# Kernel optimization log

Measured on AMD Instinct MI355X. Metric: run time of the kernel, lower is better.

The kernel has to match this reference:

```python
import jax, jax.numpy as jnp
import numpy as np

B, TAU, M, NX, NY = 256, 128, 3, 8, 8
N = NX + NY                 # 16 total sensors
D = 2 * N * N               # d_model = 512
NHEAD = 8
DFF = 2048


def _layer_norm(x, g, b, eps=1e-5):
    mu = jnp.mean(x, axis=-1, keepdims=True)
    var = jnp.mean((x - mu) ** 2, axis=-1, keepdims=True)
    return (x - mu) / jnp.sqrt(var + eps) * g + b


def _mha(x, wi, bi, wo, bo):
    Bq, S, Dm = x.shape
    hd = Dm // NHEAD
    qkv = x @ wi.T + bi                         # (B,S,3D)
    q, k, v = jnp.split(qkv, 3, axis=-1)
    sh = lambda t: t.reshape(Bq, S, NHEAD, hd).transpose(0, 2, 1, 3)
    q, k, v = sh(q), sh(k), sh(v)
    att = jax.nn.softmax(jnp.einsum('bhqd,bhkd->bhqk', q, k) / jnp.sqrt(jnp.float32(hd)), axis=-1)
    o = jnp.einsum('bhqk,bhkd->bhqd', att, v).transpose(0, 2, 1, 3).reshape(Bq, S, Dm)
    return o @ wo.T + bo


def poly_roots(c):
    # companion-matrix roots; c[..., 0] is the leading coefficient
    n = c.shape[-1] - 1
    first = (-c[..., 1:] / c[..., :1])[..., None, :]                      # (..., 1, n)
    below = jnp.broadcast_to(jnp.eye(n - 1, n, dtype=c.dtype), c.shape[:-1] + (n - 1, n))
    return jnp.linalg.eigvals(jnp.concatenate([first, below], axis=-2))   # (..., n)


def root_music_doa(Rz, m):
    # Rz: (B, n, n) Hermitian PSD (gram + eps*I) -> eigh == eig sorted by |lambda|
    n = Rz.shape[-1]
    w, v = jnp.linalg.eigh(Rz)                  # ascending real eigenvalues
    Un = v[..., : n - m]                        # noise subspace (smallest n-m)
    F = Un @ jnp.conj(jnp.swapaxes(Un, -1, -2))
    # sum of each diagonal, offsets -(n-1)..(n-1) -> 2n-1 poly coefficients
    coeffs = jnp.stack([jnp.sum(jnp.diagonal(F, offset=o, axis1=-2, axis2=-1), axis=-1)
                        for o in range(-(n - 1), n)], axis=-1)
    roots = poly_roots(coeffs)                  # (B, 2n-2)
    # sort by closeness to unit circle; push roots with |r|>=1 to the back
    keyv = jnp.abs(jnp.abs(roots) - 1.0) + jnp.where(jnp.abs(roots) < 1.0, 0.0, 1e6)
    sel = jnp.take_along_axis(roots, jnp.argsort(keyv, axis=-1)[..., :m], axis=-1)
    # dist=0.5, f=1 -> 1/(2*pi*dist*f) = 1/pi
    return jnp.arcsin(jnp.angle(sel) / jnp.pi)  # (B, m)


def setup_inputs() -> dict:
    key = jax.random.key(0)
    ks = jax.random.split(key, 12)
    rn = lambda k, s: 0.02 * jax.random.normal(k, s, jnp.float32)
    return {
        'Rx_tau': jax.random.normal(ks[0], (B, TAU, 2 * N, N), jnp.float32),
        'in_proj_w': rn(ks[1], (3 * D, D)), 'in_proj_b': jnp.zeros((3 * D,), jnp.float32),
        'out_proj_w': rn(ks[2], (D, D)), 'out_proj_b': jnp.zeros((D,), jnp.float32),
        'ln1_g': jnp.ones((D,), jnp.float32), 'ln1_b': jnp.zeros((D,), jnp.float32),
        'ffn_w1': rn(ks[3], (DFF, D)), 'ffn_b1': jnp.zeros((DFF,), jnp.float32),
        'ffn_w2': rn(ks[4], (D, DFF)), 'ffn_b2': jnp.zeros((D,), jnp.float32),
        'ln2_g': jnp.ones((D,), jnp.float32), 'ln2_b': jnp.zeros((D,), jnp.float32),
        'fcx_w': rn(ks[5], (2 * NX * NX, D)), 'fcx_b': jnp.zeros((2 * NX * NX,), jnp.float32),
        'fcy_w': rn(ks[6], (2 * NY * NY, D)), 'fcy_b': jnp.zeros((2 * NY * NY,), jnp.float32),
        'mlp_w1': rn(ks[7], (256, 2 * M)), 'mlp_b1': jnp.zeros((256,), jnp.float32),
        'mlp_w2': rn(ks[8], (256, 256)), 'mlp_b2': jnp.zeros((256,), jnp.float32),
        'mlp_w3': rn(ks[9], (2 * M, 256)), 'mlp_b3': jnp.zeros((2 * M,), jnp.float32),
    }


def reference(Rx_tau, in_proj_w, in_proj_b, out_proj_w, out_proj_b, ln1_g, ln1_b,
              ffn_w1, ffn_b1, ffn_w2, ffn_b2, ln2_g, ln2_b,
              fcx_w, fcx_b, fcy_w, fcy_b,
              mlp_w1, mlp_b1, mlp_w2, mlp_b2, mlp_w3, mlp_b3):
    x = Rx_tau.reshape(Rx_tau.shape[0], -1, D)  # (B, tau, 512)
    # post-LN TransformerEncoderLayer (eval: dropout off)
    x = _layer_norm(x + _mha(x, in_proj_w, in_proj_b, out_proj_w, out_proj_b), ln1_g, ln1_b)
    ff = jnp.maximum(x @ ffn_w1.T + ffn_b1, 0.0) @ ffn_w2.T + ffn_b2
    x = _layer_norm(x + ff, ln2_g, ln2_b)
    x = jnp.mean(x, axis=1)                     # (B, D)
    Rx = (x @ fcx_w.T + fcx_b).reshape(-1, 2 * NX, NX)
    Ry = (x @ fcy_w.T + fcy_b).reshape(-1, 2 * NY, NY)
    Kx = jax.lax.complex(Rx[:, :NX], Rx[:, NX:])
    Ky = jax.lax.complex(Ry[:, :NY], Ry[:, NY:])
    # gram_diagonal_overload: K^H K + eps*I, eps=1
    Rz_x = jnp.einsum('bji,bjk->bik', jnp.conj(Kx), Kx) + jnp.eye(NX, dtype=Kx.dtype)
    Rz_y = jnp.einsum('bji,bjk->bik', jnp.conj(Ky), Ky) + jnp.eye(NY, dtype=Ky.dtype)
    doa_t = root_music_doa(Rz_x, M)
    doa_p = root_music_doa(Rz_y, M)
    h = jnp.concatenate([doa_t, doa_p], axis=-1).astype(jnp.float32)  # (B, 2M)
    h = jnp.maximum(h @ mlp_w1.T + mlp_b1, 0.0)
    h = jnp.maximum(h @ mlp_w2.T + mlp_b2, 0.0)
    outs = h @ mlp_w3.T + mlp_b3
    return outs[:, :M], outs[:, M:]
```

## Files before the change

### kernel.cpp

```cpp
#include <hip/hip_runtime.h>
#include <math.h>

#define S_LEN 128
#define D_MODEL 512
#define B_SZ 256
#define NHEADS 8
#define HD 64
#define DFFN 2048
#define PI_D 3.14159265358979323846

typedef _Float16 f16x8 __attribute__((ext_vector_type(8)));
typedef _Float16 f16x4 __attribute__((ext_vector_type(4)));
typedef float f32x4 __attribute__((ext_vector_type(4)));

__global__ __launch_bounds__(256) void cvt_split(const float* __restrict__ in,
        _Float16* __restrict__ hi, _Float16* __restrict__ lo, int n4)
{
    const int i = blockIdx.x * 256 + threadIdx.x;
    if (i >= n4) return;
    float4 v = ((const float4*)in)[i];
    f16x4 h, l;
    _Float16 h0 = (_Float16)v.x; h[0] = h0; l[0] = (_Float16)(v.x - (float)h0);
    _Float16 h1 = (_Float16)v.y; h[1] = h1; l[1] = (_Float16)(v.y - (float)h1);
    _Float16 h2 = (_Float16)v.z; h[2] = h2; l[2] = (_Float16)(v.z - (float)h2);
    _Float16 h3 = (_Float16)v.w; h[3] = h3; l[3] = (_Float16)(v.w - (float)h3);
    ((f16x4*)hi)[i] = h;
    ((f16x4*)lo)[i] = l;
}

template<int RELU>
__global__ __launch_bounds__(256) void gemm_mfma(const float* __restrict__ A,
        const _Float16* __restrict__ Whg, const _Float16* __restrict__ Wlg,
        const float* __restrict__ bias, float* __restrict__ C,
        int M, int N, int K)
{
    __shared__ _Float16 Ah[128 * 64];
    __shared__ _Float16 Al[128 * 64];
    __shared__ _Float16 Wh[128 * 64];
    __shared__ _Float16 Wl[128 * 64];
    const int t = threadIdx.x;
    const int lane = t & 63;
    const int w = t >> 6;
    const int wr = w >> 1, wc = w & 1;
    const int row0 = blockIdx.y * 128, col0 = blockIdx.x * 128;

    const int ar = t >> 2;
    const int ak = (t & 3) * 16;
    const int wrow = t >> 1;
    const int wk = (t & 1) * 32;

    const float*    Abase = A   + (size_t)(row0 + ar) * K + ak;
    const _Float16* Whb   = Whg + (size_t)(col0 + wrow) * K + wk;
    const _Float16* Wlb   = Wlg + (size_t)(col0 + wrow) * K + wk;

    float4 aR[2][4];
    f16x8 wRh[4], wRl[4];

    auto load_tile = [&](int k0) {
#pragma unroll
        for (int s = 0; s < 2; ++s)
#pragma unroll
            for (int j = 0; j < 4; ++j)
                aR[s][j] = *(const float4*)(Abase + (size_t)s * 64 * K + k0 + 4 * j);
#pragma unroll
        for (int j = 0; j < 4; ++j) {
            wRh[j] = *(const f16x8*)(Whb + k0 + 8 * j);
            wRl[j] = *(const f16x8*)(Wlb + k0 + 8 * j);
        }
    };

    f32x4 acc[4][4];
#pragma unroll
    for (int m = 0; m < 4; ++m)
#pragma unroll
        for (int n = 0; n < 4; ++n) acc[m][n] = (f32x4)0.f;

    const int NT = K >> 6;
    load_tile(0);
    for (int kt = 0; kt < NT; ++kt) {
        __syncthreads();
#pragma unroll
        for (int s = 0; s < 2; ++s) {
            const int row = ar + s * 64;
            const int sw = (row & 7) << 3;
            f16x8 hv[2], lv[2];
#pragma unroll
            for (int j = 0; j < 4; ++j) {
                const float4 v = aR[s][j];
                f16x8& H = hv[j >> 1];
                f16x8& L = lv[j >> 1];
                const int p = (j & 1) * 4;
                _Float16 h0 = (_Float16)v.x; H[p + 0] = h0; L[p + 0] = (_Float16)(v.x - (float)h0);
                _Float16 h1 = (_Float16)v.y; H[p + 1] = h1; L[p + 1] = (_Float16)(v.y - (float)h1);
                _Float16 h2 = (_Float16)v.z; H[p + 2] = h2; L[p + 2] = (_Float16)(v.z - (float)h2);
                _Float16 h3 = (_Float16)v.w; H[p + 3] = h3; L[p + 3] = (_Float16)(v.w - (float)h3);
            }
            const int eb = row * 64;
            *(f16x8*)&Ah[eb + ((ak + 0) ^ sw)] = hv[0];
            *(f16x8*)&Ah[eb + ((ak + 8) ^ sw)] = hv[1];
            *(f16x8*)&Al[eb + ((ak + 0) ^ sw)] = lv[0];
            *(f16x8*)&Al[eb + ((ak + 8) ^ sw)] = lv[1];
        }
        {
            const int sw = (wrow & 7) << 3;
            const int eb = wrow * 64;
#pragma unroll
            for (int j = 0; j < 4; ++j) {
                *(f16x8*)&Wh[eb + ((wk + 8 * j) ^ sw)] = wRh[j];
                *(f16x8*)&Wl[eb + ((wk + 8 * j) ^ sw)] = wRl[j];
            }
        }
        __syncthreads();
        if (kt + 1 < NT) load_tile((kt + 1) << 6);
#pragma unroll
        for (int ks = 0; ks < 2; ++ks) {
            const int kf = ks * 32 + (lane >> 4) * 8;
            f16x8 afh[4], afl[4], bfh[4], bfl[4];
#pragma unroll
            for (int m = 0; m < 4; ++m) {
                const int row = wr * 64 + m * 16 + (lane & 15);
                const int e = row * 64 + (kf ^ ((row & 7) << 3));
                afh[m] = *(const f16x8*)&Ah[e];
                afl[m] = *(const f16x8*)&Al[e];
            }
#pragma unroll
            for (int n = 0; n < 4; ++n) {
                const int row = wc * 64 + n * 16 + (lane & 15);
                const int e = row * 64 + (kf ^ ((row & 7) << 3));
                bfh[n] = *(const f16x8*)&Wh[e];
                bfl[n] = *(const f16x8*)&Wl[e];
            }
#pragma unroll
            for (int m = 0; m < 4; ++m)
#pragma unroll
                for (int n = 0; n < 4; ++n) {
                    acc[m][n] = __builtin_amdgcn_mfma_f32_16x16x32_f16(afh[m], bfh[n], acc[m][n], 0, 0, 0);
                    acc[m][n] = __builtin_amdgcn_mfma_f32_16x16x32_f16(afh[m], bfl[n], acc[m][n], 0, 0, 0);
                    acc[m][n] = __builtin_amdgcn_mfma_f32_16x16x32_f16(afl[m], bfh[n], acc[m][n], 0, 0, 0);
                }
        }
    }
#pragma unroll
    for (int m = 0; m < 4; ++m) {
        const int rowc = row0 + wr * 64 + m * 16 + ((lane >> 4) << 2);
#pragma unroll
        for (int n = 0; n < 4; ++n) {
            const int colc = col0 + wc * 64 + n * 16 + (lane & 15);
            const float bv = bias[colc];
#pragma unroll
            for (int j = 0; j < 4; ++j) {
                float v = acc[m][n][j] + bv;
                if (RELU) v = fmaxf(v, 0.f);
                C[(size_t)(rowc + j) * N + colc] = v;
            }
        }
    }
}

template<int RELU>
__global__ __launch_bounds__(256) void gemm_bias(const float* __restrict__ A,
        const float* __restrict__ W, const float* __restrict__ bias,
        float* __restrict__ C, int M, int N, int K)
{
    __shared__ float As[8][128];
    __shared__ float Ws[8][128];
    const int tid = threadIdx.x;
    const int tn = tid & 15, tm = tid >> 4;
    const int row0 = blockIdx.y * 128, col0 = blockIdx.x * 128;
    const int lr = tid >> 1, lc = (tid & 1) * 4;
    const float* Ap = A + (size_t)(row0 + lr) * K + lc;
    const float* Wp = W + (size_t)(col0 + lr) * K + lc;
    float acc[8][8];
#pragma unroll
    for (int i = 0; i < 8; ++i)
#pragma unroll
        for (int j = 0; j < 8; ++j) acc[i][j] = 0.f;

    for (int k0 = 0; k0 < K; k0 += 8) {
        float4 av = *(const float4*)(Ap + k0);
        float4 wv = *(const float4*)(Wp + k0);
        __syncthreads();
        As[lc + 0][lr] = av.x; As[lc + 1][lr] = av.y;
        As[lc + 2][lr] = av.z; As[lc + 3][lr] = av.w;
        Ws[lc + 0][lr] = wv.x; Ws[lc + 1][lr] = wv.y;
        Ws[lc + 2][lr] = wv.z; Ws[lc + 3][lr] = wv.w;
        __syncthreads();
#pragma unroll
        for (int k = 0; k < 8; ++k) {
            float ar[8], wr[8];
#pragma unroll
            for (int i = 0; i < 8; ++i) ar[i] = As[k][tm * 8 + i];
#pragma unroll
            for (int j = 0; j < 8; ++j) wr[j] = Ws[k][tn * 8 + j];
#pragma unroll
            for (int i = 0; i < 8; ++i)
#pragma unroll
                for (int j = 0; j < 8; ++j)
                    acc[i][j] = fmaf(ar[i], wr[j], acc[i][j]);
        }
    }
#pragma unroll
    for (int i = 0; i < 8; ++i) {
        const int r = row0 + tm * 8 + i;
#pragma unroll
        for (int j = 0; j < 8; ++j) {
            const int c = col0 + tn * 8 + j;
            float v = acc[i][j] + bias[c];
            if (RELU) v = fmaxf(v, 0.f);
            C[(size_t)r * N + c] = v;
        }
    }
}

__global__ __launch_bounds__(128) void attn_kernel(const float* __restrict__ qkv,
                                                   float* __restrict__ o)
{
    const int bh = blockIdx.x;
    const int b = bh >> 3, hh = bh & 7;
    const int t = threadIdx.x;
    __shared__ float Ks[S_LEN][HD];
    __shared__ float Vs[S_LEN][HD];
    const float* base = qkv + (size_t)b * S_LEN * (3 * D_MODEL);
    const float* krow = base + (size_t)t * (3 * D_MODEL) + D_MODEL + hh * HD;
    const float* vrow = base + (size_t)t * (3 * D_MODEL) + 2 * D_MODEL + hh * HD;
#pragma unroll
    for (int d = 0; d < HD; d += 4) {
        *(float4*)&Ks[t][d] = *(const float4*)(krow + d);
        *(float4*)&Vs[t][d] = *(const float4*)(vrow + d);
    }
    float q[HD];
    const float* qrow = base + (size_t)t * (3 * D_MODEL) + hh * HD;
#pragma unroll
    for (int d = 0; d < HD; d += 4) {
        float4 v4 = *(const float4*)(qrow + d);
        q[d] = v4.x; q[d + 1] = v4.y; q[d + 2] = v4.z; q[d + 3] = v4.w;
    }
    __syncthreads();
    float m = -1e30f, l = 0.f;
    float oacc[HD];
#pragma unroll
    for (int d = 0; d < HD; ++d) oacc[d] = 0.f;
    for (int j = 0; j < S_LEN; ++j) {
        float s = 0.f;
#pragma unroll
        for (int d = 0; d < HD; ++d) s = fmaf(q[d], Ks[j][d], s);
        s *= 0.125f;
        const float nm = fmaxf(m, s);
        const float sc = expf(m - nm);
        const float p = expf(s - nm);
        l = l * sc + p;
#pragma unroll
        for (int d = 0; d < HD; ++d) oacc[d] = oacc[d] * sc + p * Vs[j][d];
        m = nm;
    }
    const float inv = 1.f / l;
    float* orow = o + (size_t)b * S_LEN * D_MODEL + (size_t)t * D_MODEL + hh * HD;
#pragma unroll
    for (int d = 0; d < HD; ++d) orow[d] = oacc[d] * inv;
}

__global__ __launch_bounds__(128) void add_ln_kernel(const float* __restrict__ a,
        const float* __restrict__ bb, const float* __restrict__ g,
        const float* __restrict__ be, float* __restrict__ out)
{
    __shared__ float red[2];
    const int row = blockIdx.x, t = threadIdx.x;
    float4 av = *(const float4*)(a + (size_t)row * D_MODEL + t * 4);
    float4 bv = *(const float4*)(bb + (size_t)row * D_MODEL + t * 4);
    float x0 = av.x + bv.x, x1 = av.y + bv.y, x2 = av.z + bv.z, x3 = av.w + bv.w;
    float ssum = x0 + x1 + x2 + x3;
#pragma unroll
    for (int off = 32; off >= 1; off >>= 1) ssum += __shfl_xor(ssum, off);
    if ((t & 63) == 0) red[t >> 6] = ssum;
    __syncthreads();
    const float mean = (red[0] + red[1]) * (1.f / 512.f);
    __syncthreads();
    float d0 = x0 - mean, d1 = x1 - mean, d2 = x2 - mean, d3 = x3 - mean;
    float sq = d0 * d0 + d1 * d1 + d2 * d2 + d3 * d3;
#pragma unroll
    for (int off = 32; off >= 1; off >>= 1) sq += __shfl_xor(sq, off);
    if ((t & 63) == 0) red[t >> 6] = sq;
    __syncthreads();
    const float var = (red[0] + red[1]) * (1.f / 512.f);
    const float inv = 1.0f / sqrtf(var + 1e-5f);
    float4 gv = *(const float4*)(g + t * 4);
    float4 bev = *(const float4*)(be + t * 4);
    float4 ov = make_float4(d0 * inv * gv.x + bev.x, d1 * inv * gv.y + bev.y,
                            d2 * inv * gv.z + bev.z, d3 * inv * gv.w + bev.w);
    *(float4*)(out + (size_t)row * D_MODEL + t * 4) = ov;
}

__global__ __launch_bounds__(128) void pool_kernel(const float* __restrict__ x,
                                                   float* __restrict__ pooled)
{
    const int b = blockIdx.x, t = threadIdx.x;
    float4 acc = make_float4(0.f, 0.f, 0.f, 0.f);
    const float* base = x + (size_t)b * S_LEN * D_MODEL + t * 4;
    for (int s = 0; s < S_LEN; ++s) {
        float4 v = *(const float4*)(base + (size_t)s * D_MODEL);
        acc.x += v.x; acc.y += v.y; acc.z += v.z; acc.w += v.w;
    }
    const float sc = 1.f / 128.f;
    float4 ov = make_float4(acc.x * sc, acc.y * sc, acc.z * sc, acc.w * sc);
    *(float4*)(pooled + (size_t)b * D_MODEL + t * 4) = ov;
}

__global__ __launch_bounds__(64) void music_kernel(const float* __restrict__ RxRy,
                                                   float* __restrict__ hbuf)
{
    const int pb = blockIdx.x;
    const int b = pb >> 1, which = pb & 1;
    const float* src = RxRy + (size_t)which * (B_SZ * 128) + (size_t)b * 128;
    const int t = threadIdx.x;

    __shared__ double KRe[8][8], KIm[8][8];
    __shared__ double Are[8][8], Aim[8][8];
    __shared__ double Vre[8][8], Vim[8][8];
    __shared__ double Fre[8][8], Fim[8][8];
    __shared__ double rot[4];
    __shared__ double cr[15], ci[15];
    __shared__ double br[14], bi[14];
    __shared__ double zr[14], zi[14];
    __shared__ int topidx[3];

    {
        const int i = t >> 3, j = t & 7;
        KRe[i][j] = (double)src[i * 8 + j];
        KIm[i][j] = (double)src[64 + i * 8 + j];
    }
    __syncthreads();
    {
        const int i = t >> 3, k = t & 7;
        double sre = (i == k) ? 1.0 : 0.0, sim = 0.0;
        for (int j = 0; j < 8; ++j) {
            const double ar = KRe[j][i], ai = KIm[j][i];
            const double xr = KRe[j][k], xi = KIm[j][k];
            sre += ar * xr + ai * xi;
            sim += ar * xi - ai * xr;
        }
        Are[i][k] = sre; Aim[i][k] = sim;
        Vre[i][k] = (i == k) ? 1.0 : 0.0;
        Vim[i][k] = 0.0;
    }
    __syncthreads();

    for (int sweep = 0; sweep < 9; ++sweep) {
        for (int p = 0; p < 7; ++p) {
            for (int q = p + 1; q < 8; ++q) {
                if (t == 0) {
                    const double gre = Are[p][q], gim = Aim[p][q];
                    const double r = sqrt(gre * gre + gim * gim);
                    if (r < 1e-60) {
                        rot[0] = 1.0; rot[1] = 0.0; rot[2] = 1.0; rot[3] = 0.0;
                    } else {
                        const double tau = (Are[p][p] - Are[q][q]) / (2.0 * r);
                        const double tt = ((tau >= 0.0) ? 1.0 : -1.0) /
                                          (fabs(tau) + sqrt(1.0 + tau * tau));
                        const double c = 1.0 / sqrt(1.0 + tt * tt);
                        rot[0] = c; rot[1] = tt * c; rot[2] = gre / r; rot[3] = gim / r;
                    }
                }
                __syncthreads();
                const double c = rot[0], s = rot[1], er = rot[2], ei = rot[3];
                if (t < 8) {
                    const int k = t;
                    double apr = Are[k][p], api = Aim[k][p];
                    double aqr = Are[k][q], aqi = Aim[k][q];
                    Are[k][p] = c * apr + s * (er * aqr + ei * aqi);
                    Aim[k][p] = c * api + s * (er * aqi - ei * aqr);
                    Are[k][q] = c * aqr - s * (er * apr - ei * api);
                    Aim[k][q] = c * aqi - s * (er * api + ei * apr);
                    double vpr = Vre[k][p], vpi = Vim[k][p];
                    double vqr = Vre[k][q], vqi = Vim[k][q];
                    Vre[k][p] = c * vpr + s * (er * vqr + ei * vqi);
                    Vim[k][p] = c * vpi + s * (er * vqi - ei * vqr);
                    Vre[k][q] = c * vqr - s * (er * vpr - ei * vpi);
                    Vim[k][q] = c * vqi - s * (er * vpi + ei * vpr);
                }
                __syncthreads();
                if (t < 8) {
                    const int k = t;
                    double apr = Are[p][k], api = Aim[p][k];
                    double aqr = Are[q][k], aqi = Aim[q][k];
                    Are[p][k] = c * apr + s * (er * aqr - ei * aqi);
                    Aim[p][k] = c * api + s * (er * aqi + ei * aqr);
                    Are[q][k] = c * aqr - s * (er * apr + ei * api);
                    Aim[q][k] = c * aqi - s * (er * api - ei * apr);
                }
                __syncthreads();
                if (t == 0) {
                    Are[p][q] = 0.0; Aim[p][q] = 0.0;
                    Are[q][p] = 0.0; Aim[q][p] = 0.0;
                    Aim[p][p] = 0.0; Aim[q][q] = 0.0;
                }
                __syncthreads();
            }
        }
    }

    if (t == 0) {
        bool used[8] = {false, false, false, false, false, false, false, false};
        for (int tt = 0; tt < 3; ++tt) {
            double best = -1e300; int bidx = 0;
            for (int i = 0; i < 8; ++i)
                if (!used[i] && Are[i][i] > best) { best = Are[i][i]; bidx = i; }
            used[bidx] = true; topidx[tt] = bidx;
        }
    }
    __syncthreads();
    {
        const int i = t >> 3, j = t & 7;
        double fre = (i == j) ? 1.0 : 0.0, fim = 0.0;
        for (int tt = 0; tt < 3; ++tt) {
            const int e = topidx[tt];
            const double vir = Vre[i][e], vii = Vim[i][e];
            const double vjr = Vre[j][e], vji = Vim[j][e];
            fre -= vir * vjr + vii * vji;
            fim -= vii * vjr - vir * vji;
        }
        Fre[i][j] = fre; Fim[i][j] = fim;
    }
    __syncthreads();
    if (t < 15) {
        const int o = t - 7;
        double sre = 0.0, sim = 0.0;
        for (int r = 0; r < 8; ++r) {
            const int cc = r + o;
            if (cc >= 0 && cc < 8) { sre += Fre[r][cc]; sim += Fim[r][cc]; }
        }
        cr[t] = sre; ci[t] = sim;
    }
    __syncthreads();
    if (t < 14) {
        const double den = cr[0] * cr[0] + ci[0] * ci[0];
        const double nr = cr[t + 1], ni = ci[t + 1];
        br[t] = (nr * cr[0] + ni * ci[0]) / den;
        bi[t] = (ni * cr[0] - nr * ci[0]) / den;
        double zre_ = 1.0, zim_ = 0.0;
        for (int k = 0; k <= t; ++k) {
            const double a2 = zre_ * 0.4 - zim_ * 0.9;
            zim_ = zre_ * 0.9 + zim_ * 0.4;
            zre_ = a2;
        }
        zr[t] = zre_; zi[t] = zim_;
    }
    __syncthreads();
    for (int it = 0; it < 128; ++it) {
        double nzr = 0.0, nzi = 0.0;
        if (t < 14) {
            const double zre_ = zr[t], zim_ = zi[t];
            double wre = 1.0, wim = 0.0;
            for (int j = 0; j < 14; ++j) {
                const double tr = wre * zre_ - wim * zim_ + br[j];
                wim = wre * zim_ + wim * zre_ + bi[j];
                wre = tr;
            }
            double dre = 1.0, dim = 0.0;
            for (int j = 0; j < 14; ++j) {
                if (j == t) continue;
                const double exr = zre_ - zr[j], exi = zim_ - zi[j];
                const double tr = dre * exr - dim * exi;
                dim = dre * exi + dim * exr;
                dre = tr;
            }
            const double dd = dre * dre + dim * dim;
            if (dd > 1e-260) {
                const double qre = (wre * dre + wim * dim) / dd;
                const double qim = (wim * dre - wre * dim) / dd;
                nzr = zre_ - qre; nzi = zim_ - qim;
            } else {
                nzr = zre_ + 1e-8; nzi = zim_ - 1e-8;
            }
        }
        __syncthreads();
        if (t < 14) { zr[t] = nzr; zi[t] = nzi; }
        __syncthreads();
    }
    if (t == 0) {
        double keyv[14]; bool used[14];
        for (int i = 0; i < 14; ++i) {
            const double mag = sqrt(zr[i] * zr[i] + zi[i] * zi[i]);
            keyv[i] = fabs(mag - 1.0) + ((mag < 1.0) ? 0.0 : 1e6);
            used[i] = false;
        }
        for (int tt = 0; tt < 3; ++tt) {
            double best = 1e300; int bidx = 0;
            for (int i = 0; i < 14; ++i)
                if (!used[i] && keyv[i] < best) { best = keyv[i]; bidx = i; }
            used[bidx] = true;
            const double ang = atan2(zi[bidx], zr[bidx]);
            double ratio = ang / PI_D;
            if (ratio > 1.0) ratio = 1.0;
            if (ratio < -1.0) ratio = -1.0;
            hbuf[(size_t)b * 6 + which * 3 + tt] = (float)asin(ratio);
        }
    }
}

__global__ __launch_bounds__(256) void mlp_kernel(const float* __restrict__ hbuf,
        const float* __restrict__ w1, const float* __restrict__ b1,
        const float* __restrict__ w2, const float* __restrict__ b2,
        const float* __restrict__ w3, const float* __restrict__ b3,
        float* __restrict__ outp)
{
    const int b = blockIdx.x, t = threadIdx.x;
    __shared__ float hin[8];
    __shared__ float h1[256];
    __shared__ float h2[256];
    if (t < 6) hin[t] = hbuf[b * 6 + t];
    __syncthreads();
    float acc = b1[t];
#pragma unroll
    for (int k = 0; k < 6; ++k) acc += hin[k] * w1[t * 6 + k];
    h1[t] = fmaxf(acc, 0.f);
    __syncthreads();
    float acc2 = b2[t];
    for (int k = 0; k < 256; ++k) acc2 += h1[k] * w2[t * 256 + k];
    h2[t] = fmaxf(acc2, 0.f);
    __syncthreads();
    if (t < 6) {
        float acc3 = b3[t];
        for (int k = 0; k < 256; ++k) acc3 += h2[k] * w3[t * 256 + k];
        if (t < 3) outp[b * 3 + t] = acc3;
        else       outp[B_SZ * 3 + b * 3 + (t - 3)] = acc3;
    }
}

extern "C" void kernel_launch(void* const* d_in, const int* in_sizes, int n_in,
                              void* d_out, int out_size, void* d_ws, size_t ws_size,
                              hipStream_t stream)
{
    const float* x_in      = (const float*)d_in[0];
    const float* in_proj_w = (const float*)d_in[1];
    const float* in_proj_b = (const float*)d_in[2];
    const float* out_proj_w= (const float*)d_in[3];
    const float* out_proj_b= (const float*)d_in[4];
    const float* ln1_g     = (const float*)d_in[5];
    const float* ln1_b     = (const float*)d_in[6];
    const float* ffn_w1    = (const float*)d_in[7];
    const float* ffn_b1    = (const float*)d_in[8];
    const float* ffn_w2    = (const float*)d_in[9];
    const float* ffn_b2    = (const float*)d_in[10];
    const float* ln2_g     = (const float*)d_in[11];
    const float* ln2_b     = (const float*)d_in[12];
    const float* fcx_w     = (const float*)d_in[13];
    const float* fcx_b     = (const float*)d_in[14];
    const float* fcy_w     = (const float*)d_in[15];
    const float* fcy_b     = (const float*)d_in[16];
    const float* mlp_w1    = (const float*)d_in[17];
    const float* mlp_b1    = (const float*)d_in[18];
    const float* mlp_w2    = (const float*)d_in[19];
    const float* mlp_b2    = (const float*)d_in[20];
    const float* mlp_w3    = (const float*)d_in[21];
    const float* mlp_b3    = (const float*)d_in[22];

    const size_t N_IPW = 1536 * 512, N_OPW = 512 * 512;
    const size_t N_F1W = 2048 * 512, N_F2W = 512 * 2048;
    const size_t WCVT = (N_IPW + N_OPW + N_F1W + N_F2W);
    float* ws = (float*)d_ws;
    _Float16* ipw_h = (_Float16*)ws;
    _Float16* ipw_l = ipw_h + N_IPW;
    _Float16* opw_h = ipw_l + N_IPW;
    _Float16* opw_l = opw_h + N_OPW;
    _Float16* f1w_h = opw_l + N_OPW;
    _Float16* f1w_l = f1w_h + N_F1W;
    _Float16* f2w_h = f1w_l + N_F1W;
    _Float16* f2w_l = f2w_h + N_F2W;
    float* dyn = ws + WCVT;

    const size_t ws_floats = ws_size / sizeof(float);
    int c = 256;
    while (c > 1 && (size_t)393216 * (size_t)c + 262144 + WCVT > ws_floats) c >>= 1;

    float* RA     = dyn;
    float* x1     = RA + (size_t)262144 * c;
    float* ff2    = x1 + (size_t)65536 * c;
    float* pooled = ff2 + (size_t)65536 * c;
    float* RxRy   = pooled + 131072;
    float* hbuf   = RxRy + 65536;

    float* qkv = RA;
    float* o   = RA + (size_t)196608 * c;
    float* ff1 = RA;

    cvt_split<<<(N_IPW / 4 + 255) / 256, 256, 0, stream>>>(in_proj_w,  ipw_h, ipw_l, N_IPW / 4);
    cvt_split<<<(N_OPW / 4 + 255) / 256, 256, 0, stream>>>(out_proj_w, opw_h, opw_l, N_OPW / 4);
    cvt_split<<<(N_F1W / 4 + 255) / 256, 256, 0, stream>>>(ffn_w1,     f1w_h, f1w_l, N_F1W / 4);
    cvt_split<<<(N_F2W / 4 + 255) / 256, 256, 0, stream>>>(ffn_w2,     f2w_h, f2w_l, N_F2W / 4);

    for (int b0 = 0; b0 < B_SZ; b0 += c) {
        const int Tc = c * S_LEN;
        const float* xc = x_in + (size_t)b0 * S_LEN * D_MODEL;

        gemm_mfma<0><<<dim3(1536 / 128, Tc / 128), 256, 0, stream>>>(
            xc, ipw_h, ipw_l, in_proj_b, qkv, Tc, 3 * D_MODEL, D_MODEL);
        attn_kernel<<<c * NHEADS, 128, 0, stream>>>(qkv, o);
        gemm_mfma<0><<<dim3(512 / 128, Tc / 128), 256, 0, stream>>>(
            o, opw_h, opw_l, out_proj_b, x1, Tc, D_MODEL, D_MODEL);
        add_ln_kernel<<<Tc, 128, 0, stream>>>(xc, x1, ln1_g, ln1_b, x1);
        gemm_mfma<1><<<dim3(DFFN / 128, Tc / 128), 256, 0, stream>>>(
            x1, f1w_h, f1w_l, ffn_b1, ff1, Tc, DFFN, D_MODEL);
        gemm_mfma<0><<<dim3(512 / 128, Tc / 128), 256, 0, stream>>>(
            ff1, f2w_h, f2w_l, ffn_b2, ff2, Tc, D_MODEL, DFFN);
        add_ln_kernel<<<Tc, 128, 0, stream>>>(x1, ff2, ln2_g, ln2_b, x1);
        pool_kernel<<<c, 128, 0, stream>>>(x1, pooled + (size_t)b0 * D_MODEL);
    }

    gemm_bias<0><<<dim3(1, 2), 256, 0, stream>>>(
        pooled, fcx_w, fcx_b, RxRy, B_SZ, 128, D_MODEL);
    gemm_bias<0><<<dim3(1, 2), 256, 0, stream>>>(
        pooled, fcy_w, fcy_b, RxRy + B_SZ * 128, B_SZ, 128, D_MODEL);
    music_kernel<<<2 * B_SZ, 64, 0, stream>>>(RxRy, hbuf);
    mlp_kernel<<<B_SZ, 256, 0, stream>>>(hbuf, mlp_w1, mlp_b1, mlp_w2, mlp_b2,
                                         mlp_w3, mlp_b3, (float*)d_out);
}
```

Measured before the change: 1.723 ms.

## Pre-split activations to fp16 hi/lo and stream GEMM tiles via async LDS loads

```diff
diff --git a/kernel.cpp b/kernel.cpp
--- a/kernel.cpp
+++ b/kernel.cpp
@@ -12,6 +12,12 @@
 typedef _Float16 f16x8 __attribute__((ext_vector_type(8)));
 typedef _Float16 f16x4 __attribute__((ext_vector_type(4)));
 typedef float f32x4 __attribute__((ext_vector_type(4)));
+
+__device__ __forceinline__ void gl_lds(const _Float16* g, _Float16* l) {
+    __builtin_amdgcn_global_load_lds(
+        (const __attribute__((address_space(1))) void*)g,
+        (__attribute__((address_space(3))) void*)l, 16, 0, 0);
+}
 
 __global__ __launch_bounds__(256) void cvt_split(const float* __restrict__ in,
         _Float16* __restrict__ hi, _Float16* __restrict__ lo, int n4)
@@ -28,44 +34,45 @@
     ((f16x4*)lo)[i] = l;
 }
 
-template<int RELU>
-__global__ __launch_bounds__(256) void gemm_mfma(const float* __restrict__ A,
+template<int OUTMODE>
+__global__ __launch_bounds__(256) void gemm_mfma(
+        const _Float16* __restrict__ Ahg, const _Float16* __restrict__ Alg,
         const _Float16* __restrict__ Whg, const _Float16* __restrict__ Wlg,
-        const float* __restrict__ bias, float* __restrict__ C,
+        const float* __restrict__ bias, float* __restrict__ Cf,
+        _Float16* __restrict__ Ch, _Float16* __restrict__ Cl,
         int M, int N, int K)
 {
-    __shared__ _Float16 Ah[128 * 64];
-    __shared__ _Float16 Al[128 * 64];
-    __shared__ _Float16 Wh[128 * 64];
-    __shared__ _Float16 Wl[128 * 64];
+    __shared__ _Float16 lds[2][4][8192];
     const int t = threadIdx.x;
     const int lane = t & 63;
     const int w = t >> 6;
     const int wr = w >> 1, wc = w & 1;
     const int row0 = blockIdx.y * 128, col0 = blockIdx.x * 128;
 
-    const int ar = t >> 2;
-    const int ak = (t & 3) * 16;
-    const int wrow = t >> 1;
-    const int wk = (t & 1) * 32;
-
-    const float*    Abase = A   + (size_t)(row0 + ar) * K + ak;
-    const _Float16* Whb   = Whg + (size_t)(col0 + wrow) * K + wk;
-    const _Float16* Wlb   = Wlg + (size_t)(col0 + wrow) * K + wk;
-
-    float4 aR[2][4];
-    f16x8 wRh[4], wRl[4];
-
-    auto load_tile = [&](int k0) {
-#pragma unroll
-        for (int s = 0; s < 2; ++s)
-#pragma unroll
-            for (int j = 0; j < 4; ++j)
-                aR[s][j] = *(const float4*)(Abase + (size_t)s * 64 * K + k0 + 4 * j);
-#pragma unroll
-        for (int j = 0; j < 4; ++j) {
-            wRh[j] = *(const f16x8*)(Whb + k0 + 8 * j);
-            wRl[j] = *(const f16x8*)(Wlb + k0 + 8 * j);
+    const int srow = lane >> 3;
+    const int schunk = (lane & 7) ^ srow;
+
+    const _Float16* gA[2] = { Ahg, Alg };
+    const _Float16* gW[2] = { Whg, Wlg };
+
+    auto stage = [&](int buf, int kt) {
+        const int k0 = kt << 6;
+#pragma unroll
+        for (int a = 0; a < 2; ++a) {
+#pragma unroll
+            for (int j = 0; j < 4; ++j) {
+                const int i = w * 4 + j;
+                const int rA = row0 + 8 * i + srow;
+                gl_lds(gA[a] + (size_t)rA * K + k0 + schunk * 8,
+                       &lds[buf][a][i * 512]);
+            }
+#pragma unroll
+            for (int j = 0; j < 4; ++j) {
+                const int i = w * 4 + j;
+                const int rW = col0 + 8 * i + srow;
+                gl_lds(gW[a] + (size_t)rW * K + k0 + schunk * 8,
+                       &lds[buf][2 + a][i * 512]);
+            }
         }
     };
 
@@ -76,42 +83,20 @@
         for (int n = 0; n < 4; ++n) acc[m][n] = (f32x4)0.f;
 
     const int NT = K >> 6;
-    load_tile(0);
+    stage(0, 0);
+    float bv[4];
+#pragma unroll
+    for (int n = 0; n < 4; ++n) bv[n] = bias[col0 + wc * 64 + n * 16 + (lane & 15)];
+
     for (int kt = 0; kt < NT; ++kt) {
-        __syncthreads();
-#pragma unroll
-        for (int s = 0; s < 2; ++s) {
-            const int row = ar + s * 64;
-            const int sw = (row & 7) << 3;
-            f16x8 hv[2], lv[2];
-#pragma unroll
-            for (int j = 0; j < 4; ++j) {
-                const float4 v = aR[s][j];
-                f16x8& H = hv[j >> 1];
-                f16x8& L = lv[j >> 1];
-                const int p = (j & 1) * 4;
-                _Float16 h0 = (_Float16)v.x; H[p + 0] = h0; L[p + 0] = (_Float16)(v.x - (float)h0);
-                _Float16 h1 = (_Float16)v.y; H[p + 1] = h1; L[p + 1] = (_Float16)(v.y - (float)h1);
-                _Float16 h2 = (_Float16)v.z; H[p + 2] = h2; L[p + 2] = (_Float16)(v.z - (float)h2);
-                _Float16 h3 = (_Float16)v.w; H[p + 3] = h3; L[p + 3] = (_Float16)(v.w - (float)h3);
-            }
-            const int eb = row * 64;
-            *(f16x8*)&Ah[eb + ((ak + 0) ^ sw)] = hv[0];
-            *(f16x8*)&Ah[eb + ((ak + 8) ^ sw)] = hv[1];
-            *(f16x8*)&Al[eb + ((ak + 0) ^ sw)] = lv[0];
-            *(f16x8*)&Al[eb + ((ak + 8) ^ sw)] = lv[1];
-        }
-        {
-            const int sw = (wrow & 7) << 3;
-            const int eb = wrow * 64;
-#pragma unroll
-            for (int j = 0; j < 4; ++j) {
-                *(f16x8*)&Wh[eb + ((wk + 8 * j) ^ sw)] = wRh[j];
-                *(f16x8*)&Wl[eb + ((wk + 8 * j) ^ sw)] = wRl[j];
-            }
-        }
-        __syncthreads();
-        if (kt + 1 < NT) load_tile((kt + 1) << 6);
+        const int cur = kt & 1;
+        if (kt + 1 < NT) {
+            stage(cur ^ 1, kt + 1);
+            asm volatile("s_waitcnt vmcnt(16)" ::: "memory");
+        } else {
+            asm volatile("s_waitcnt vmcnt(0)" ::: "memory");
+        }
+        __syncthreads();
 #pragma unroll
         for (int ks = 0; ks < 2; ++ks) {
             const int kf = ks * 32 + (lane >> 4) * 8;
@@ -120,15 +105,15 @@
             for (int m = 0; m < 4; ++m) {
                 const int row = wr * 64 + m * 16 + (lane & 15);
                 const int e = row * 64 + (kf ^ ((row & 7) << 3));
-                afh[m] = *(const f16x8*)&Ah[e];
-                afl[m] = *(const f16x8*)&Al[e];
+                afh[m] = *(const f16x8*)&lds[cur][0][e];
+                afl[m] = *(const f16x8*)&lds[cur][1][e];
             }
 #pragma unroll
             for (int n = 0; n < 4; ++n) {
                 const int row = wc * 64 + n * 16 + (lane & 15);
                 const int e = row * 64 + (kf ^ ((row & 7) << 3));
-                bfh[n] = *(const f16x8*)&Wh[e];
-                bfl[n] = *(const f16x8*)&Wl[e];
+                bfh[n] = *(const f16x8*)&lds[cur][2][e];
+                bfl[n] = *(const f16x8*)&lds[cur][3][e];
             }
 #pragma unroll
             for (int m = 0; m < 4; ++m)
@@ -139,19 +124,27 @@
                     acc[m][n] = __builtin_amdgcn_mfma_f32_16x16x32_f16(afl[m], bfh[n], acc[m][n], 0, 0, 0);
                 }
         }
-    }
+        __syncthreads();
+    }
+
 #pragma unroll
     for (int m = 0; m < 4; ++m) {
         const int rowc = row0 + wr * 64 + m * 16 + ((lane >> 4) << 2);
 #pragma unroll
         for (int n = 0; n < 4; ++n) {
             const int colc = col0 + wc * 64 + n * 16 + (lane & 15);
-            const float bv = bias[colc];
 #pragma unroll
             for (int j = 0; j < 4; ++j) {
-                float v = acc[m][n][j] + bv;
-                if (RELU) v = fmaxf(v, 0.f);
-                C[(size_t)(rowc + j) * N + colc] = v;
+                float v = acc[m][n][j] + bv[n];
+                if (OUTMODE == 2) {
+                    v = fmaxf(v, 0.f);
+                    const size_t idx = (size_t)(rowc + j) * N + colc;
+                    _Float16 h = (_Float16)v;
+                    Ch[idx] = h;
+                    Cl[idx] = (_Float16)(v - (float)h);
+                } else {
+                    Cf[(size_t)(rowc + j) * N + colc] = v;
+                }
             }
         }
     }
@@ -187,16 +180,16 @@
         __syncthreads();
 #pragma unroll
         for (int k = 0; k < 8; ++k) {
-            float ar[8], wr[8];
+            float ar[8], wrg[8];
 #pragma unroll
             for (int i = 0; i < 8; ++i) ar[i] = As[k][tm * 8 + i];
 #pragma unroll
-            for (int j = 0; j < 8; ++j) wr[j] = Ws[k][tn * 8 + j];
+            for (int j = 0; j < 8; ++j) wrg[j] = Ws[k][tn * 8 + j];
 #pragma unroll
             for (int i = 0; i < 8; ++i)
 #pragma unroll
                 for (int j = 0; j < 8; ++j)
-                    acc[i][j] = fmaf(ar[i], wr[j], acc[i][j]);
+                    acc[i][j] = fmaf(ar[i], wrg[j], acc[i][j]);
         }
     }
 #pragma unroll
@@ -213,7 +206,7 @@
 }
 
 __global__ __launch_bounds__(128) void attn_kernel(const float* __restrict__ qkv,
-                                                   float* __restrict__ o)
+        _Float16* __restrict__ oh, _Float16* __restrict__ ol)
 {
     const int bh = blockIdx.x;
     const int b = bh >> 3, hh = bh & 7;
@@ -254,14 +247,21 @@
         m = nm;
     }
     const float inv = 1.f / l;
-    float* orow = o + (size_t)b * S_LEN * D_MODEL + (size_t)t * D_MODEL + hh * HD;
-#pragma unroll
-    for (int d = 0; d < HD; ++d) orow[d] = oacc[d] * inv;
-}
-
+    const size_t ob = (size_t)b * S_LEN * D_MODEL + (size_t)t * D_MODEL + hh * HD;
+#pragma unroll
+    for (int d = 0; d < HD; ++d) {
+        const float v = oacc[d] * inv;
+        const _Float16 h = (_Float16)v;
+        oh[ob + d] = h;
+        ol[ob + d] = (_Float16)(v - (float)h);
+    }
+}
+
+template<int SPLIT>
 __global__ __launch_bounds__(128) void add_ln_kernel(const float* __restrict__ a,
         const float* __restrict__ bb, const float* __restrict__ g,
-        const float* __restrict__ be, float* __restrict__ out)
+        const float* __restrict__ be, float* __restrict__ out,
+        _Float16* __restrict__ oh, _Float16* __restrict__ ol)
 {
     __shared__ float red[2];
     const int row = blockIdx.x, t = threadIdx.x;
@@ -288,6 +288,15 @@
     float4 ov = make_float4(d0 * inv * gv.x + bev.x, d1 * inv * gv.y + bev.y,
                             d2 * inv * gv.z + bev.z, d3 * inv * gv.w + bev.w);
     *(float4*)(out + (size_t)row * D_MODEL + t * 4) = ov;
+    if (SPLIT) {
+        f16x4 h, l;
+        _Float16 h0 = (_Float16)ov.x; h[0] = h0; l[0] = (_Float16)(ov.x - (float)h0);
+        _Float16 h1 = (_Float16)ov.y; h[1] = h1; l[1] = (_Float16)(ov.y - (float)h1);
+        _Float16 h2 = (_Float16)ov.z; h[2] = h2; l[2] = (_Float16)(ov.z - (float)h2);
+        _Float16 h3 = (_Float16)ov.w; h[3] = h3; l[3] = (_Float16)(ov.w - (float)h3);
+        *(f16x4*)&oh[(size_t)row * D_MODEL + t * 4] = h;
+        *(f16x4*)&ol[(size_t)row * D_MODEL + t * 4] = l;
+    }
 }
 
 __global__ __launch_bounds__(128) void pool_kernel(const float* __restrict__ x,
@@ -312,109 +321,117 @@
     const int b = pb >> 1, which = pb & 1;
     const float* src = RxRy + (size_t)which * (B_SZ * 128) + (size_t)b * 128;
     const int t = threadIdx.x;
+    const int i = t >> 3, j = t & 7;
 
     __shared__ double KRe[8][8], KIm[8][8];
-    __shared__ double Are[8][8], Aim[8][8];
-    __shared__ double Vre[8][8], Vim[8][8];
+    __shared__ double Ar[8][8], Ai[8][8], Vr[8][8], Vi[8][8];
     __shared__ double Fre[8][8], Fim[8][8];
-    __shared__ double rot[4];
-    __shared__ double cr[15], ci[15];
-    __shared__ double br[14], bi[14];
-    __shared__ double zr[14], zi[14];
+    __shared__ double rc[4], rs[4], rer[4], rei[4];
+    __shared__ double cr[15], ci[15], br[14], bi[14], zr[14], zi[14];
     __shared__ int topidx[3];
 
+    KRe[i][j] = (double)src[i * 8 + j];
+    KIm[i][j] = (double)src[64 + i * 8 + j];
+    __syncthreads();
     {
-        const int i = t >> 3, j = t & 7;
-        KRe[i][j] = (double)src[i * 8 + j];
-        KIm[i][j] = (double)src[64 + i * 8 + j];
-    }
-    __syncthreads();
-    {
-        const int i = t >> 3, k = t & 7;
-        double sre = (i == k) ? 1.0 : 0.0, sim = 0.0;
-        for (int j = 0; j < 8; ++j) {
-            const double ar = KRe[j][i], ai = KIm[j][i];
-            const double xr = KRe[j][k], xi = KIm[j][k];
+        double sre = (i == j) ? 1.0 : 0.0, sim = 0.0;
+        for (int r = 0; r < 8; ++r) {
+            const double ar = KRe[r][i], ai = KIm[r][i];
+            const double xr = KRe[r][j], xi = KIm[r][j];
             sre += ar * xr + ai * xi;
             sim += ar * xi - ai * xr;
         }
-        Are[i][k] = sre; Aim[i][k] = sim;
-        Vre[i][k] = (i == k) ? 1.0 : 0.0;
-        Vim[i][k] = 0.0;
-    }
-    __syncthreads();
-
-    for (int sweep = 0; sweep < 9; ++sweep) {
-        for (int p = 0; p < 7; ++p) {
-            for (int q = p + 1; q < 8; ++q) {
-                if (t == 0) {
-                    const double gre = Are[p][q], gim = Aim[p][q];
-                    const double r = sqrt(gre * gre + gim * gim);
-                    if (r < 1e-60) {
-                        rot[0] = 1.0; rot[1] = 0.0; rot[2] = 1.0; rot[3] = 0.0;
-                    } else {
-                        const double tau = (Are[p][p] - Are[q][q]) / (2.0 * r);
-                        const double tt = ((tau >= 0.0) ? 1.0 : -1.0) /
-                                          (fabs(tau) + sqrt(1.0 + tau * tau));
-                        const double c = 1.0 / sqrt(1.0 + tt * tt);
-                        rot[0] = c; rot[1] = tt * c; rot[2] = gre / r; rot[3] = gim / r;
-                    }
-                }
-                __syncthreads();
-                const double c = rot[0], s = rot[1], er = rot[2], ei = rot[3];
-                if (t < 8) {
-                    const int k = t;
-                    double apr = Are[k][p], api = Aim[k][p];
-                    double aqr = Are[k][q], aqi = Aim[k][q];
-                    Are[k][p] = c * apr + s * (er * aqr + ei * aqi);
-                    Aim[k][p] = c * api + s * (er * aqi - ei * aqr);
-                    Are[k][q] = c * aqr - s * (er * apr - ei * api);
-                    Aim[k][q] = c * aqi - s * (er * api + ei * apr);
-                    double vpr = Vre[k][p], vpi = Vim[k][p];
-                    double vqr = Vre[k][q], vqi = Vim[k][q];
-                    Vre[k][p] = c * vpr + s * (er * vqr + ei * vqi);
-                    Vim[k][p] = c * vpi + s * (er * vqi - ei * vqr);
-                    Vre[k][q] = c * vqr - s * (er * vpr - ei * vpi);
-                    Vim[k][q] = c * vqi - s * (er * vpi + ei * vpr);
-                }
-                __syncthreads();
-                if (t < 8) {
-                    const int k = t;
-                    double apr = Are[p][k], api = Aim[p][k];
-                    double aqr = Are[q][k], aqi = Aim[q][k];
-                    Are[p][k] = c * apr + s * (er * aqr - ei * aqi);
-                    Aim[p][k] = c * api + s * (er * aqi + ei * aqr);
-                    Are[q][k] = c * aqr - s * (er * apr + ei * api);
-                    Aim[q][k] = c * aqi - s * (er * api - ei * apr);
-                }
-                __syncthreads();
-                if (t == 0) {
-                    Are[p][q] = 0.0; Aim[p][q] = 0.0;
-                    Are[q][p] = 0.0; Aim[q][p] = 0.0;
-                    Aim[p][p] = 0.0; Aim[q][q] = 0.0;
-                }
-                __syncthreads();
-            }
-        }
+        Ar[i][j] = sre; Ai[i][j] = sim;
+        Vr[i][j] = (i == j) ? 1.0 : 0.0;
+        Vi[i][j] = 0.0;
+    }
+    __syncthreads();
+
+    for (int sw = 0; sw < 9; ++sw)
+    for (int rr = 0; rr < 7; ++rr) {
+        int pp[4], qq[4];
+        pp[0] = 0;                 qq[0] = (rr + 6) % 7 + 1;
+        pp[1] = rr % 7 + 1;        qq[1] = (rr + 5) % 7 + 1;
+        pp[2] = (rr + 1) % 7 + 1;  qq[2] = (rr + 4) % 7 + 1;
+        pp[3] = (rr + 2) % 7 + 1;  qq[3] = (rr + 3) % 7 + 1;
+        if (t < 4) {
+            const int p = pp[t], q = qq[t];
+            const double gre = Ar[p][q], gim = Ai[p][q];
+            const double r = sqrt(gre * gre + gim * gim);
+            double c, s, er, ei;
+            if (r < 1e-60) { c = 1.0; s = 0.0; er = 1.0; ei = 0.0; }
+            else {
+                const double tau = (Ar[p][p] - Ar[q][q]) / (2.0 * r);
+                const double tt = ((tau >= 0.0) ? 1.0 : -1.0) /
+                                  (fabs(tau) + sqrt(1.0 + tau * tau));
+                c = 1.0 / sqrt(1.0 + tt * tt); s = tt * c;
+                er = gre / r; ei = gim / r;
+            }
+            rc[t] = c; rs[t] = s; rer[t] = er; rei[t] = ei;
+        }
+        __syncthreads();
+        int gi = 0, gj = 0;
+#pragma unroll
+        for (int g = 0; g < 4; ++g) {
+            if (pp[g] == i || qq[g] == i) gi = g;
+            if (pp[g] == j || qq[g] == j) gj = g;
+        }
+        const int ri_q = (qq[gi] == i), rj_q = (qq[gj] == j);
+        const double ci_ = rc[gi], si_ = rs[gi], eir = rer[gi], eii = rei[gi];
+        const double cj_ = rc[gj], sj_ = rs[gj], ejr = rer[gj], eji = rei[gj];
+        const int Pi = pp[gi], Qi = qq[gi], Pj = pp[gj], Qj = qq[gj];
+
+        double bPr, bPi_, bQr, bQi_;
+        {
+            double apr = Ar[Pi][Pj], api = Ai[Pi][Pj];
+            double aqr = Ar[Pi][Qj], aqi = Ai[Pi][Qj];
+            if (!rj_q) { bPr = cj_ * apr + sj_ * (ejr * aqr + eji * aqi);
+                         bPi_= cj_ * api + sj_ * (ejr * aqi - eji * aqr); }
+            else       { bPr = cj_ * aqr - sj_ * (ejr * apr - eji * api);
+                         bPi_= cj_ * aqi - sj_ * (ejr * api + eji * apr); }
+            apr = Ar[Qi][Pj]; api = Ai[Qi][Pj];
+            aqr = Ar[Qi][Qj]; aqi = Ai[Qi][Qj];
+            if (!rj_q) { bQr = cj_ * apr + sj_ * (ejr * aqr + eji * aqi);
+                         bQi_= cj_ * api + sj_ * (ejr * aqi - eji * aqr); }
+            else       { bQr = cj_ * aqr - sj_ * (ejr * apr - eji * api);
+                         bQi_= cj_ * aqi - sj_ * (ejr * api + eji * apr); }
+        }
+        double nAr, nAi_;
+        if (!ri_q) { nAr = ci_ * bPr + si_ * (eir * bQr - eii * bQi_);
+                     nAi_= ci_ * bPi_+ si_ * (eir * bQi_ + eii * bQr); }
+        else       { nAr = ci_ * bQr - si_ * (eir * bPr + eii * bPi_);
+                     nAi_= ci_ * bQi_- si_ * (eir * bPi_ - eii * bPr); }
+        double nVr, nVi_;
+        {
+            const double vpr = Vr[i][Pj], vpi = Vi[i][Pj];
+            const double vqr = Vr[i][Qj], vqi = Vi[i][Qj];
+            if (!rj_q) { nVr = cj_ * vpr + sj_ * (ejr * vqr + eji * vqi);
+                         nVi_= cj_ * vpi + sj_ * (ejr * vqi - eji * vqr); }
+            else       { nVr = cj_ * vqr - sj_ * (ejr * vpr - eji * vpi);
+                         nVi_= cj_ * vqi - sj_ * (ejr * vpi + eji * vpr); }
+        }
+        __syncthreads();
+        Ar[i][j] = nAr; Ai[i][j] = nAi_;
+        Vr[i][j] = nVr; Vi[i][j] = nVi_;
+        __syncthreads();
     }
 
     if (t == 0) {
         bool used[8] = {false, false, false, false, false, false, false, false};
         for (int tt = 0; tt < 3; ++tt) {
             double best = -1e300; int bidx = 0;
-            for (int i = 0; i < 8; ++i)
-                if (!used[i] && Are[i][i] > best) { best = Are[i][i]; bidx = i; }
+            for (int k = 0; k < 8; ++k)
+                if (!used[k] && Ar[k][k] > best) { best = Ar[k][k]; bidx = k; }
             used[bidx] = true; topidx[tt] = bidx;
         }
     }
     __syncthreads();
     {
-        const int i = t >> 3, j = t & 7;
         double fre = (i == j) ? 1.0 : 0.0, fim = 0.0;
         for (int tt = 0; tt < 3; ++tt) {
             const int e = topidx[tt];
-            const double vir = Vre[i][e], vii = Vim[i][e];
-            const double vjr = Vre[j][e], vji = Vim[j][e];
+            const double vir = Vr[i][e], vii = Vi[i][e];
+            const double vjr = Vr[j][e], vji = Vi[j][e];
             fre -= vir * vjr + vii * vji;
             fim -= vii * vjr - vir * vji;
         }
@@ -450,15 +467,15 @@
         if (t < 14) {
             const double zre_ = zr[t], zim_ = zi[t];
             double wre = 1.0, wim = 0.0;
-            for (int j = 0; j < 14; ++j) {
-                const double tr = wre * zre_ - wim * zim_ + br[j];
-                wim = wre * zim_ + wim * zre_ + bi[j];
+            for (int k = 0; k < 14; ++k) {
+                const double tr = wre * zre_ - wim * zim_ + br[k];
+                wim = wre * zim_ + wim * zre_ + bi[k];
                 wre = tr;
             }
             double dre = 1.0, dim = 0.0;
-            for (int j = 0; j < 14; ++j) {
-                if (j == t) continue;
-                const double exr = zre_ - zr[j], exi = zim_ - zi[j];
+            for (int k = 0; k < 14; ++k) {
+                if (k == t) continue;
+                const double exr = zre_ - zr[k], exi = zim_ - zi[k];
                 const double tr = dre * exr - dim * exi;
                 dim = dre * exi + dim * exr;
                 dre = tr;
@@ -478,15 +495,15 @@
     }
     if (t == 0) {
         double keyv[14]; bool used[14];
-        for (int i = 0; i < 14; ++i) {
-            const double mag = sqrt(zr[i] * zr[i] + zi[i] * zi[i]);
-            keyv[i] = fabs(mag - 1.0) + ((mag < 1.0) ? 0.0 : 1e6);
-            used[i] = false;
+        for (int k = 0; k < 14; ++k) {
+            const double mag = sqrt(zr[k] * zr[k] + zi[k] * zi[k]);
+            keyv[k] = fabs(mag - 1.0) + ((mag < 1.0) ? 0.0 : 1e6);
+            used[k] = false;
         }
         for (int tt = 0; tt < 3; ++tt) {
             double best = 1e300; int bidx = 0;
-            for (int i = 0; i < 14; ++i)
-                if (!used[i] && keyv[i] < best) { best = keyv[i]; bidx = i; }
+            for (int k = 0; k < 14; ++k)
+                if (!used[k] && keyv[k] < best) { best = keyv[k]; bidx = k; }
             used[bidx] = true;
             const double ang = atan2(zi[bidx], zr[bidx]);
             double ratio = ang / PI_D;
@@ -556,7 +573,7 @@
 
     const size_t N_IPW = 1536 * 512, N_OPW = 512 * 512;
     const size_t N_F1W = 2048 * 512, N_F2W = 512 * 2048;
-    const size_t WCVT = (N_IPW + N_OPW + N_F1W + N_F2W);
+    const size_t WCVT = N_IPW + N_OPW + N_F1W + N_F2W;
     float* ws = (float*)d_ws;
     _Float16* ipw_h = (_Float16*)ws;
     _Float16* ipw_l = ipw_h + N_IPW;
@@ -570,18 +587,28 @@
 
     const size_t ws_floats = ws_size / sizeof(float);
     int c = 256;
-    while (c > 1 && (size_t)393216 * (size_t)c + 262144 + WCVT > ws_floats) c >>= 1;
-
-    float* RA     = dyn;
-    float* x1     = RA + (size_t)262144 * c;
-    float* ff2    = x1 + (size_t)65536 * c;
+    while (c > 1 && (size_t)524288 * (size_t)c + 262144 + WCVT > ws_floats) c >>= 1;
+
+    float* R0     = dyn;
+    float* xhf    = R0 + (size_t)262144 * c;
+    float* xlf    = xhf + (size_t)32768 * c;
+    float* x1     = xlf + (size_t)32768 * c;
+    float* x1hf   = x1 + (size_t)65536 * c;
+    float* x1lf   = x1hf + (size_t)32768 * c;
+    float* ff2    = x1lf + (size_t)32768 * c;
     float* pooled = ff2 + (size_t)65536 * c;
     float* RxRy   = pooled + 131072;
     float* hbuf   = RxRy + 65536;
 
-    float* qkv = RA;
-    float* o   = RA + (size_t)196608 * c;
-    float* ff1 = RA;
+    float*    qkv  = R0;
+    _Float16* oh   = (_Float16*)(R0 + (size_t)196608 * c);
+    _Float16* ol   = oh + (size_t)65536 * c;
+    _Float16* ff1h = (_Float16*)R0;
+    _Float16* ff1l = ff1h + (size_t)262144 * c;
+    _Float16* xh   = (_Float16*)xhf;
+    _Float16* xl   = (_Float16*)xlf;
+    _Float16* x1h  = (_Float16*)x1hf;
+    _Float16* x1l  = (_Float16*)x1lf;
 
     cvt_split<<<(N_IPW / 4 + 255) / 256, 256, 0, stream>>>(in_proj_w,  ipw_h, ipw_l, N_IPW / 4);
     cvt_split<<<(N_OPW / 4 + 255) / 256, 256, 0, stream>>>(out_proj_w, opw_h, opw_l, N_OPW / 4);
@@ -591,18 +618,20 @@
     for (int b0 = 0; b0 < B_SZ; b0 += c) {
         const int Tc = c * S_LEN;
         const float* xc = x_in + (size_t)b0 * S_LEN * D_MODEL;
-
+        const int n4x = Tc * D_MODEL / 4;
+
+        cvt_split<<<(n4x + 255) / 256, 256, 0, stream>>>(xc, xh, xl, n4x);
         gemm_mfma<0><<<dim3(1536 / 128, Tc / 128), 256, 0, stream>>>(
-            xc, ipw_h, ipw_l, in_proj_b, qkv, Tc, 3 * D_MODEL, D_MODEL);
-        attn_kernel<<<c * NHEADS, 128, 0, stream>>>(qkv, o);
+            xh, xl, ipw_h, ipw_l, in_proj_b, qkv, nullptr, nullptr, Tc, 3 * D_MODEL, D_MODEL);
+        attn_kernel<<<c * NHEADS, 128, 0, stream>>>(qkv, oh, ol);
         gemm_mfma<0><<<dim3(512 / 128, Tc / 128), 256, 0, stream>>>(
-            o, opw_h, opw_l, out_proj_b, x1, Tc, D_MODEL, D_MODEL);
-        add_ln_kernel<<<Tc, 128, 0, stream>>>(xc, x1, ln1_g, ln1_b, x1);
-        gemm_mfma<1><<<dim3(DFFN / 128, Tc / 128), 256, 0, stream>>>(
-            x1, f1w_h, f1w_l, ffn_b1, ff1, Tc, DFFN, D_MODEL);
+            oh, ol, opw_h, opw_l, out_proj_b, x1, nullptr, nullptr, Tc, D_MODEL, D_MODEL);
+        add_ln_kernel<1><<<Tc, 128, 0, stream>>>(xc, x1, ln1_g, ln1_b, x1, x1h, x1l);
+        gemm_mfma<2><<<dim3(DFFN / 128, Tc / 128), 256, 0, stream>>>(
+            x1h, x1l, f1w_h, f1w_l, ffn_b1, nullptr, ff1h, ff1l, Tc, DFFN, D_MODEL);
         gemm_mfma<0><<<dim3(512 / 128, Tc / 128), 256, 0, stream>>>(
-            ff1, f2w_h, f2w_l, ffn_b2, ff2, Tc, D_MODEL, DFFN);
-        add_ln_kernel<<<Tc, 128, 0, stream>>>(x1, ff2, ln2_g, ln2_b, x1);
+            ff1h, ff1l, f2w_h, f2w_l, ffn_b2, ff2, nullptr, nullptr, Tc, D_MODEL, DFFN);
+        add_ln_kernel<0><<<Tc, 128, 0, stream>>>(x1, ff2, ln2_g, ln2_b, x1, nullptr, nullptr);
         pool_kernel<<<c, 128, 0, stream>>>(x1, pooled + (size_t)b0 * D_MODEL);
     }
 
```

Result: slower. 1.821 ms (+5.7%).
